# Performance work log

Hardware: AMD Instinct MI355X
Metric: run time of the kernel (lower is better)

## Reference

```python
import jax, jax.numpy as jnp
import numpy as np

NUM_EXPERTS = 8
EMBED_DIM = 1024
BATCH, SEQ = 4, 2048


def setup_inputs() -> dict:
    key = jax.random.key(0)
    k1, k2, k3 = jax.random.split(key, 3)
    E_symb = jax.random.normal(k1, (BATCH, SEQ, EMBED_DIM), dtype=jnp.float32)
    gate_w = jax.random.normal(k2, (EMBED_DIM, NUM_EXPERTS), dtype=jnp.float32) * 0.02
    gate_b = jnp.zeros((NUM_EXPERTS,), dtype=jnp.float32)
    expert_w = jax.random.normal(k3, (NUM_EXPERTS, EMBED_DIM, EMBED_DIM), dtype=jnp.float32) * 0.02
    return {"E_symb": E_symb, "gate_w": gate_w, "gate_b": gate_b,
            "expert_w": expert_w, "k": 2}


def reference(E_symb, gate_w, gate_b, expert_w, k):
    B, S, D = E_symb.shape
    E = expert_w.shape[0]
    x = E_symb.reshape(-1, D)                       # [T, D]
    logits = x @ gate_w + gate_b                    # [T, E]
    probs = jax.nn.softmax(logits.astype(jnp.float32), axis=-1)
    # top-k selection; NOTE: original renormalizes routing_weights but never
    # applies them to expert outputs -> combine is an UNWEIGHTED sum.
    _, sel = jax.lax.top_k(probs, k)                # [T, k]
    mask = jax.nn.one_hot(sel, E, dtype=x.dtype).sum(axis=1)  # [T, E] in {0,1}
    # dense grouped-GEMM then masked combine (replaces per-expert gather/scatter loop)
    y = jnp.einsum('td,edf->tef', x, expert_w)      # [T, E, D]
    out = jnp.einsum('tef,te->tf', y, mask)         # [T, D]
    return out.reshape(B, S, D)
```

## Files before the change

### kernel.cpp

```cpp
#include <hip/hip_runtime.h>
#include <hip/hip_bf16.h>
#include <stdint.h>

#define T_TOK 8192
#define DIM   1024
#define NEXP  8
#define BM    128
#define BN    128
#define BK2   32

typedef __bf16 bf16_t;
typedef bf16_t bf16x8 __attribute__((ext_vector_type(8)));
typedef bf16_t bf16x4 __attribute__((ext_vector_type(4)));
typedef float  f32x4  __attribute__((ext_vector_type(4)));

#define WS_CNT    0
#define CIDX(p)   ((p) << 4)
#define WS_LIST   8192
#define WS_XBF    (4u << 20)
#define WS_W2     (20u << 20)
#define WS_NEED_PSUM ((size_t)76 << 20)

__device__ const int d_PA[28] = {0,0,0,0,0,0,0,1,1,1,1,1,1,2,2,2,2,2,3,3,3,3,4,4,4,5,5,6};
__device__ const int d_PB[28] = {1,2,3,4,5,6,7,2,3,4,5,6,7,3,4,5,6,7,4,5,6,7,5,6,7,6,7,7};

__device__ __forceinline__ void gload16(const void* g, void* l) {
    __builtin_amdgcn_global_load_lds(
        (const __attribute__((address_space(1))) unsigned int*)g,
        (__attribute__((address_space(3))) unsigned int*)l, 16, 0, 0);
}

__device__ __forceinline__ int swz32(int r, int k) {
    return ((r * BK2 + k) * 2) ^ (((r >> 1) & 3) << 4);
}

#define WAITCNT_VM0()   do { asm volatile("s_waitcnt vmcnt(0)" ::: "memory"); \
                             __builtin_amdgcn_sched_barrier(0); } while (0)
#define WAITCNT_VM4()   do { asm volatile("s_waitcnt vmcnt(4)" ::: "memory"); \
                             __builtin_amdgcn_sched_barrier(0); } while (0)
#define WAITCNT_LGKM0() do { asm volatile("s_waitcnt lgkmcnt(0)" ::: "memory"); \
                             __builtin_amdgcn_sched_barrier(0); } while (0)
#define BARRIER()       do { __builtin_amdgcn_s_barrier(); \
                             __builtin_amdgcn_sched_barrier(0); } while (0)

__global__ void zero_cnt(int4* cnt4) {
    cnt4[threadIdx.x] = int4{0, 0, 0, 0};
}

__global__ __launch_bounds__(256) void pre1(const float* __restrict__ x,
                                            const float* __restrict__ gw,
                                            const float* __restrict__ gb,
                                            const float* __restrict__ ew,
                                            bf16_t* __restrict__ xbf,
                                            bf16_t* __restrict__ wt,
                                            int* __restrict__ cnt,
                                            int* __restrict__ list) {
    __shared__ __align__(16) float sh[NEXP * DIM];
    int bx  = blockIdx.x;
    int tid = threadIdx.x;
    if (bx < 1024) {
        float4 gb0 = *(const float4*)gb;
        float4 gb1 = *(const float4*)(gb + 4);
        float gbl[8] = {gb0.x, gb0.y, gb0.z, gb0.w, gb1.x, gb1.y, gb1.z, gb1.w};
        float* gwt = sh;
        const float4* gw4 = (const float4*)gw;
        #pragma unroll
        for (int i = 0; i < 8; i++) {
            int f4 = tid + i * 256;
            float4 v = gw4[f4];
            int d  = f4 >> 1;
            int e0 = (f4 & 1) * 4;
            gwt[(e0 + 0) * DIM + d] = v.x;
            gwt[(e0 + 1) * DIM + d] = v.y;
            gwt[(e0 + 2) * DIM + d] = v.z;
            gwt[(e0 + 3) * DIM + d] = v.w;
        }
        __syncthreads();
        int wid  = tid >> 6;
        int lane = tid & 63;
        const float4* gwt4 = (const float4*)gwt;
        for (int tt = 0; tt < 2; tt++) {
            int t = bx * 8 + wid * 2 + tt;
            const float4* xr4 = (const float4*)(x + (size_t)t * DIM);
            float acc[NEXP] = {};
            #pragma unroll
            for (int j = 0; j < 4; j++) {
                int c4 = j * 64 + lane;
                float4 v = xr4[c4];
                bf16x4 b;
                b[0] = (bf16_t)v.x; b[1] = (bf16_t)v.y;
                b[2] = (bf16_t)v.z; b[3] = (bf16_t)v.w;
                *(bf16x4*)(xbf + (size_t)t * DIM + c4 * 4) = b;
                #pragma unroll
                for (int e = 0; e < NEXP; e++) {
                    float4 g = gwt4[e * 256 + c4];
                    acc[e] += v.x * g.x + v.y * g.y + v.z * g.z + v.w * g.w;
                }
            }
            for (int off = 32; off >= 1; off >>= 1)
                #pragma unroll
                for (int e = 0; e < NEXP; e++)
                    acc[e] += __shfl_xor(acc[e], off, 64);
            if (lane == 0) {
                float logit[NEXP];
                #pragma unroll
                for (int e = 0; e < NEXP; e++) logit[e] = acc[e] + gbl[e];
                int b1 = 0; float best = logit[0];
                for (int e = 1; e < NEXP; e++) if (logit[e] > best) { best = logit[e]; b1 = e; }
                int b2 = -1; float best2 = -3.0e38f;
                for (int e = 0; e < NEXP; e++) {
                    if (e == b1) continue;
                    if (logit[e] > best2) { best2 = logit[e]; b2 = e; }
                }
                int a = min(b1, b2), bb = max(b1, b2);
                int p = a * 8 + bb;
                int pos = atomicAdd(&cnt[CIDX(p)], 1);
                list[p * T_TOK + pos] = t;
            }
        }
    } else {
        int bz  = bx - 1024;
        int g   = bz >> 8;
        int rem = bz & 255;
        int f0  = (rem & 15) * 64;
        int d0  = (rem >> 4) * 64;
        float (*tile)[65] = (float (*)[65])sh;
        const float* s1 = ew + ((size_t)g * DIM + d0) * DIM + f0;
        int fl = (tid & 15) * 4;
        int dl = tid >> 4;
        #pragma unroll
        for (int i = 0; i < 4; i++) {
            int d = dl + i * 16;
            float4 u = *(const float4*)(s1 + (size_t)d * DIM + fl);
            tile[d][fl + 0] = u.x; tile[d][fl + 1] = u.y;
            tile[d][fl + 2] = u.z; tile[d][fl + 3] = u.w;
        }
        __syncthreads();
        bf16_t* dst = wt + ((size_t)g * DIM + f0) * DIM + d0;
        int dl2 = (tid & 7) * 8;
        int fl2 = tid >> 3;
        #pragma unroll
        for (int i = 0; i < 2; i++) {
            int f = fl2 + i * 32;
            bf16x8 o;
            #pragma unroll
            for (int c = 0; c < 8; c++) o[c] = (bf16_t)tile[dl2 + c][f];
            *(bf16x8*)(dst + (size_t)f * DIM + dl2) = o;
        }
    }
}

__global__ __launch_bounds__(256) void pairsum(const bf16_t* __restrict__ wt,
                                               bf16_t* __restrict__ wsum) {
    int bz = blockIdx.x;
    int pk = bz >> 7;
    int cx = bz & 127;
    int tid = threadIdx.x;
    const bf16x8* wa = (const bf16x8*)(wt + (size_t)d_PA[pk] * DIM * DIM);
    const bf16x8* wb = (const bf16x8*)(wt + (size_t)d_PB[pk] * DIM * DIM);
    bf16x8*       wo = (bf16x8*)(wsum + (size_t)pk * DIM * DIM);
    int base = cx * 1024 + tid;
    #pragma unroll
    for (int it = 0; it < 4; it++) {
        int c = base + it * 256;
        bf16x8 u = wa[c], v = wb[c], o;
        #pragma unroll
        for (int i = 0; i < 8; i++) o[i] = (bf16_t)((float)u[i] + (float)v[i]);
        wo[c] = o;
    }
}

template <int PSUM>
__global__ __launch_bounds__(256, 4) void moe_gemm(const bf16_t* __restrict__ xbf,
                                                   const bf16_t* __restrict__ wsrc,
                                                   const int* __restrict__ cnt,
                                                   const int* __restrict__ list,
                                                   float* __restrict__ out) {
    __shared__ __align__(16) bf16_t As[2][BM * BK2];
    __shared__ __align__(16) bf16_t Bs[2][BN * BK2];
    __shared__ int toks[BM];
    __shared__ int s_desc[128];
    __shared__ int s_ntile;
    int tid  = threadIdx.x;
    int lane = tid & 63;
    int wv   = tid >> 6;
    int wm   = wv >> 1, wn = wv & 1;

    if (tid < 64) {
        int c  = cnt[CIDX(tid)];
        int tp = (c + BM - 1) >> 7;
        int pre = 0, tot = 0;
        for (int i = 0; i < 64; i++) {
            int v = __shfl(tp, i, 64);
            if (i < tid) pre += v;
            tot += v;
        }
        for (int j = 0; j < tp; j++)
            s_desc[pre + j] = tid | ((j * BM) << 8);
        if (tid == 0) s_ntile = tot;
    }
    __syncthreads();
    int nwork = s_ntile * (DIM / BN);
    int q = nwork >> 3, r = nwork & 7;
    int xcd  = blockIdx.x & 7;
    int slot = blockIdx.x >> 3;
    int share = q + (xcd < r ? 1 : 0);
    if (slot >= share) return;
    int w = xcd * q + min(xcd, r) + slot;

    int dsc = s_desc[w >> 3];
    int n0  = (w & 7) * BN;
    int p   = dsc & 63;
    int m0  = dsc >> 8;
    int e1  = p >> 3, e2 = p & 7;
    int cp  = cnt[CIDX(p)];
    int valid = min(BM, cp - m0);
    if (tid < BM) toks[tid] = list[p * T_TOK + m0 + min(tid, valid - 1)];
    __syncthreads();

    const bf16_t* asrc[2];
    #pragma unroll
    for (int i = 0; i < 2; i++) {
        int c = i * 256 + tid;
        int rr = c >> 2, js = (c & 3) ^ ((rr >> 1) & 3);
        asrc[i] = xbf + (size_t)toks[rr] * DIM + js * 8;
    }

    f32x4 acc[4][4] = {};
    int lr = lane & 15;
    int lk = (lane >> 4) * 8;

    if (PSUM) {
        const bf16_t* bsrc[2];
        int pk = e1 * 7 - (e1 * (e1 - 1)) / 2 + (e2 - e1 - 1);
        const bf16_t* bb = wsrc + (size_t)pk * DIM * DIM;
        #pragma unroll
        for (int i = 0; i < 2; i++) {
            int c = i * 256 + tid;
            int rr = c >> 2, js = (c & 3) ^ ((rr >> 1) & 3);
            bsrc[i] = bb + (size_t)(n0 + rr) * DIM + js * 8;
        }
        #pragma unroll
        for (int i = 0; i < 2; i++)
            gload16(asrc[i], &As[0][(i * 256 + wv * 64) * 8]);
        #pragma unroll
        for (int i = 0; i < 2; i++)
            gload16(bsrc[i], &Bs[0][(i * 256 + wv * 64) * 8]);

        for (int ks = 0; ks < DIM / BK2; ks++) {
            int cur = ks & 1;
            if (ks < DIM / BK2 - 1) {
                int k1 = (ks + 1) * BK2;
                #pragma unroll
                for (int i = 0; i < 2; i++)
                    gload16(asrc[i] + k1, &As[cur ^ 1][(i * 256 + wv * 64) * 8]);
                #pragma unroll
                for (int i = 0; i < 2; i++)
                    gload16(bsrc[i] + k1, &Bs[cur ^ 1][(i * 256 + wv * 64) * 8]);
                WAITCNT_VM4();
            } else {
                WAITCNT_VM0();
            }
            BARRIER();
            const char* Ab = (const char*)As[cur];
            const char* Bb = (const char*)Bs[cur];
            bf16x8 af[4], bfr[4];
            #pragma unroll
            for (int mf = 0; mf < 4; mf++)
                af[mf] = *(const bf16x8*)(Ab + swz32(wm * 64 + mf * 16 + lr, lk));
            #pragma unroll
            for (int nf = 0; nf < 4; nf++)
                bfr[nf] = *(const bf16x8*)(Bb + swz32(wn * 64 + nf * 16 + lr, lk));
            #pragma unroll
            for (int mf = 0; mf < 4; mf++)
                #pragma unroll
                for (int nf = 0; nf < 4; nf++)
                    acc[mf][nf] = __builtin_amdgcn_mfma_f32_16x16x32_bf16(
                        af[mf], bfr[nf], acc[mf][nf], 0, 0, 0);
            BARRIER();
        }
    } else {
        const bf16_t* wt1 = wsrc + (size_t)e1 * DIM * DIM;
        const bf16_t* wt2 = wsrc + (size_t)e2 * DIM * DIM;
        for (int ks = 0; ks < DIM / BK2; ks++) {
            int k0 = ks * BK2;
            #pragma unroll
            for (int i = 0; i < 2; i++)
                gload16(asrc[i] + k0, &As[0][(i * 256 + wv * 64) * 8]);
            #pragma unroll
            for (int i = 0; i < 2; i++) {
                int c = i * 256 + tid;
                int f = c >> 2, j = c & 3;
                const bf16_t* s1 = wt1 + (size_t)(n0 + f) * DIM + k0 + j * 8;
                const bf16_t* s2 = wt2 + (size_t)(n0 + f) * DIM + k0 + j * 8;
                bf16x8 u = *(const bf16x8*)s1, w2v = *(const bf16x8*)s2, o;
                #pragma unroll
                for (int t = 0; t < 8; t++) o[t] = (bf16_t)((float)u[t] + (float)w2v[t]);
                *(bf16x8*)((char*)Bs[0] + swz32(f, j * 8)) = o;
            }
            WAITCNT_LGKM0();
            WAITCNT_VM0();
            BARRIER();
            const char* Ab = (const char*)As[0];
            const char* Bb = (const char*)Bs[0];
            bf16x8 af[4], bfr[4];
            #pragma unroll
            for (int mf = 0; mf < 4; mf++)
                af[mf] = *(const bf16x8*)(Ab + swz32(wm * 64 + mf * 16 + lr, lk));
            #pragma unroll
            for (int nf = 0; nf < 4; nf++)
                bfr[nf] = *(const bf16x8*)(Bb + swz32(wn * 64 + nf * 16 + lr, lk));
            #pragma unroll
            for (int mf = 0; mf < 4; mf++)
                #pragma unroll
                for (int nf = 0; nf < 4; nf++)
                    acc[mf][nf] = __builtin_amdgcn_mfma_f32_16x16x32_bf16(
                        af[mf], bfr[nf], acc[mf][nf], 0, 0, 0);
            BARRIER();
        }
    }

    #pragma unroll
    for (int mf = 0; mf < 4; mf++) {
        #pragma unroll
        for (int reg = 0; reg < 4; reg++) {
            int rl = wm * 64 + mf * 16 + (lane >> 4) * 4 + reg;
            if (rl < valid) {
                size_t trow = (size_t)toks[rl] * DIM;
                #pragma unroll
                for (int nf = 0; nf < 4; nf++)
                    out[trow + n0 + wn * 64 + nf * 16 + lr] = acc[mf][nf][reg];
            }
        }
    }
}

extern "C" void kernel_launch(void* const* d_in, const int* in_sizes, int n_in,
                              void* d_out, int out_size, void* d_ws, size_t ws_size,
                              hipStream_t stream) {
    const float* x  = (const float*)d_in[0];
    const float* gw = (const float*)d_in[1];
    const float* gb = (const float*)d_in[2];
    const float* ew = (const float*)d_in[3];
    float* out = (float*)d_out;
    char* ws = (char*)d_ws;
    int*    cnt  = (int*)(ws + WS_CNT);
    int*    list = (int*)(ws + WS_LIST);
    bf16_t* xbf  = (bf16_t*)(ws + WS_XBF);
    bf16_t* w2   = (bf16_t*)(ws + WS_W2);
    bool psum = (ws_size >= WS_NEED_PSUM);

    zero_cnt<<<dim3(1), 256, 0, stream>>>((int4*)cnt);
    if (psum) {
        bf16_t* wt_tmp = (bf16_t*)d_out;
        pre1<<<dim3(3072), 256, 0, stream>>>(x, gw, gb, ew, xbf, wt_tmp, cnt, list);
        pairsum<<<dim3(3584), 256, 0, stream>>>(wt_tmp, w2);
        moe_gemm<1><<<dim3(1024), 256, 0, stream>>>(xbf, w2, cnt, list, out);
    } else {
        pre1<<<dim3(3072), 256, 0, stream>>>(x, gw, gb, ew, xbf, w2, cnt, list);
        moe_gemm<0><<<dim3(1024), 256, 0, stream>>>(xbf, w2, cnt, list, out);
    }
}
```

Before: 71.77 us.

## Drop precomputed pair-sum weights; run two MFMA passes per expert in GEMM

Removes the pairsum kernel that built 28 summed expert-weight matrices. The GEMM now streams both experts' weight tiles via async global-to-LDS loads into separate double buffers and issues MFMAs against each. This saves a launch and about 56 MB of pair-sum write traffic, but doubles MFMA work and B-tile loads in the GEMM. It also raises LDS use and lowers the occupancy hint from 4 to 3 blocks.

```diff
diff --git a/kernel.cpp b/kernel.cpp
--- a/kernel.cpp
+++ b/kernel.cpp
@@ -18,11 +18,7 @@
 #define CIDX(p)   ((p) << 4)
 #define WS_LIST   8192
 #define WS_XBF    (4u << 20)
-#define WS_W2     (20u << 20)
-#define WS_NEED_PSUM ((size_t)76 << 20)
-
-__device__ const int d_PA[28] = {0,0,0,0,0,0,0,1,1,1,1,1,1,2,2,2,2,2,3,3,3,3,4,4,4,5,5,6};
-__device__ const int d_PB[28] = {1,2,3,4,5,6,7,2,3,4,5,6,7,3,4,5,6,7,4,5,6,7,5,6,7,6,7,7};
+#define WS_WT     (20u << 20)
 
 __device__ __forceinline__ void gload16(const void* g, void* l) {
     __builtin_amdgcn_global_load_lds(
@@ -36,9 +32,7 @@
 
 #define WAITCNT_VM0()   do { asm volatile("s_waitcnt vmcnt(0)" ::: "memory"); \
                              __builtin_amdgcn_sched_barrier(0); } while (0)
-#define WAITCNT_VM4()   do { asm volatile("s_waitcnt vmcnt(4)" ::: "memory"); \
-                             __builtin_amdgcn_sched_barrier(0); } while (0)
-#define WAITCNT_LGKM0() do { asm volatile("s_waitcnt lgkmcnt(0)" ::: "memory"); \
+#define WAITCNT_VM6()   do { asm volatile("s_waitcnt vmcnt(6)" ::: "memory"); \
                              __builtin_amdgcn_sched_barrier(0); } while (0)
 #define BARRIER()       do { __builtin_amdgcn_s_barrier(); \
                              __builtin_amdgcn_sched_barrier(0); } while (0)
@@ -150,34 +144,14 @@
     }
 }
 
-__global__ __launch_bounds__(256) void pairsum(const bf16_t* __restrict__ wt,
-                                               bf16_t* __restrict__ wsum) {
-    int bz = blockIdx.x;
-    int pk = bz >> 7;
-    int cx = bz & 127;
-    int tid = threadIdx.x;
-    const bf16x8* wa = (const bf16x8*)(wt + (size_t)d_PA[pk] * DIM * DIM);
-    const bf16x8* wb = (const bf16x8*)(wt + (size_t)d_PB[pk] * DIM * DIM);
-    bf16x8*       wo = (bf16x8*)(wsum + (size_t)pk * DIM * DIM);
-    int base = cx * 1024 + tid;
-    #pragma unroll
-    for (int it = 0; it < 4; it++) {
-        int c = base + it * 256;
-        bf16x8 u = wa[c], v = wb[c], o;
-        #pragma unroll
-        for (int i = 0; i < 8; i++) o[i] = (bf16_t)((float)u[i] + (float)v[i]);
-        wo[c] = o;
-    }
-}
-
-template <int PSUM>
-__global__ __launch_bounds__(256, 4) void moe_gemm(const bf16_t* __restrict__ xbf,
-                                                   const bf16_t* __restrict__ wsrc,
-                                                   const int* __restrict__ cnt,
-                                                   const int* __restrict__ list,
-                                                   float* __restrict__ out) {
+__global__ __launch_bounds__(256, 3) void moe_gemm2(const bf16_t* __restrict__ xbf,
+                                                    const bf16_t* __restrict__ wt,
+                                                    const int* __restrict__ cnt,
+                                                    const int* __restrict__ list,
+                                                    float* __restrict__ out) {
     __shared__ __align__(16) bf16_t As[2][BM * BK2];
-    __shared__ __align__(16) bf16_t Bs[2][BN * BK2];
+    __shared__ __align__(16) bf16_t B1[2][BN * BK2];
+    __shared__ __align__(16) bf16_t B2[2][BN * BK2];
     __shared__ int toks[BM];
     __shared__ int s_desc[128];
     __shared__ int s_ntile;
@@ -218,106 +192,71 @@
     if (tid < BM) toks[tid] = list[p * T_TOK + m0 + min(tid, valid - 1)];
     __syncthreads();
 
-    const bf16_t* asrc[2];
+    const bf16_t *asrc[2], *b1src[2], *b2src[2];
+    const bf16_t* w1 = wt + (size_t)e1 * DIM * DIM;
+    const bf16_t* w2 = wt + (size_t)e2 * DIM * DIM;
     #pragma unroll
     for (int i = 0; i < 2; i++) {
         int c = i * 256 + tid;
         int rr = c >> 2, js = (c & 3) ^ ((rr >> 1) & 3);
-        asrc[i] = xbf + (size_t)toks[rr] * DIM + js * 8;
+        asrc[i]  = xbf + (size_t)toks[rr] * DIM + js * 8;
+        b1src[i] = w1 + (size_t)(n0 + rr) * DIM + js * 8;
+        b2src[i] = w2 + (size_t)(n0 + rr) * DIM + js * 8;
     }
 
     f32x4 acc[4][4] = {};
     int lr = lane & 15;
     int lk = (lane >> 4) * 8;
 
-    if (PSUM) {
-        const bf16_t* bsrc[2];
-        int pk = e1 * 7 - (e1 * (e1 - 1)) / 2 + (e2 - e1 - 1);
-        const bf16_t* bb = wsrc + (size_t)pk * DIM * DIM;
-        #pragma unroll
-        for (int i = 0; i < 2; i++) {
-            int c = i * 256 + tid;
-            int rr = c >> 2, js = (c & 3) ^ ((rr >> 1) & 3);
-            bsrc[i] = bb + (size_t)(n0 + rr) * DIM + js * 8;
-        }
-        #pragma unroll
-        for (int i = 0; i < 2; i++)
-            gload16(asrc[i], &As[0][(i * 256 + wv * 64) * 8]);
-        #pragma unroll
-        for (int i = 0; i < 2; i++)
-            gload16(bsrc[i], &Bs[0][(i * 256 + wv * 64) * 8]);
-
-        for (int ks = 0; ks < DIM / BK2; ks++) {
-            int cur = ks & 1;
-            if (ks < DIM / BK2 - 1) {
-                int k1 = (ks + 1) * BK2;
-                #pragma unroll
-                for (int i = 0; i < 2; i++)
-                    gload16(asrc[i] + k1, &As[cur ^ 1][(i * 256 + wv * 64) * 8]);
-                #pragma unroll
-                for (int i = 0; i < 2; i++)
-                    gload16(bsrc[i] + k1, &Bs[cur ^ 1][(i * 256 + wv * 64) * 8]);
-                WAITCNT_VM4();
-            } else {
-                WAITCNT_VM0();
-            }
-            BARRIER();
-            const char* Ab = (const char*)As[cur];
-            const char* Bb = (const char*)Bs[cur];
-            bf16x8 af[4], bfr[4];
-            #pragma unroll
-            for (int mf = 0; mf < 4; mf++)
-                af[mf] = *(const bf16x8*)(Ab + swz32(wm * 64 + mf * 16 + lr, lk));
+    #pragma unroll
+    for (int i = 0; i < 2; i++) {
+        int lds = (i * 256 + wv * 64) * 8;
+        gload16(asrc[i],  &As[0][lds]);
+        gload16(b1src[i], &B1[0][lds]);
+        gload16(b2src[i], &B2[0][lds]);
+    }
+
+    for (int ks = 0; ks < DIM / BK2; ks++) {
+        int cur = ks & 1;
+        if (ks < DIM / BK2 - 1) {
+            int k1 = (ks + 1) * BK2;
+            #pragma unroll
+            for (int i = 0; i < 2; i++) {
+                int lds = (i * 256 + wv * 64) * 8;
+                gload16(asrc[i] + k1,  &As[cur ^ 1][lds]);
+                gload16(b1src[i] + k1, &B1[cur ^ 1][lds]);
+                gload16(b2src[i] + k1, &B2[cur ^ 1][lds]);
+            }
+            WAITCNT_VM6();
+        } else {
+            WAITCNT_VM0();
+        }
+        BARRIER();
+        const char* Ab  = (const char*)As[cur];
+        const char* B1b = (const char*)B1[cur];
+        const char* B2b = (const char*)B2[cur];
+        bf16x8 af[4], b1f[4], b2f[4];
+        #pragma unroll
+        for (int mf = 0; mf < 4; mf++)
+            af[mf] = *(const bf16x8*)(Ab + swz32(wm * 64 + mf * 16 + lr, lk));
+        #pragma unroll
+        for (int nf = 0; nf < 4; nf++) {
+            b1f[nf] = *(const bf16x8*)(B1b + swz32(wn * 64 + nf * 16 + lr, lk));
+            b2f[nf] = *(const bf16x8*)(B2b + swz32(wn * 64 + nf * 16 + lr, lk));
+        }
+        #pragma unroll
+        for (int mf = 0; mf < 4; mf++)
             #pragma unroll
             for (int nf = 0; nf < 4; nf++)
-                bfr[nf] = *(const bf16x8*)(Bb + swz32(wn * 64 + nf * 16 + lr, lk));
-            #pragma unroll
-            for (int mf = 0; mf < 4; mf++)
-                #pragma unroll
-                for (int nf = 0; nf < 4; nf++)
-                    acc[mf][nf] = __builtin_amdgcn_mfma_f32_16x16x32_bf16(
-                        af[mf], bfr[nf], acc[mf][nf], 0, 0, 0);
-            BARRIER();
-        }
-    } else {
-        const bf16_t* wt1 = wsrc + (size_t)e1 * DIM * DIM;
-        const bf16_t* wt2 = wsrc + (size_t)e2 * DIM * DIM;
-        for (int ks = 0; ks < DIM / BK2; ks++) {
-            int k0 = ks * BK2;
-            #pragma unroll
-            for (int i = 0; i < 2; i++)
-                gload16(asrc[i] + k0, &As[0][(i * 256 + wv * 64) * 8]);
-            #pragma unroll
-            for (int i = 0; i < 2; i++) {
-                int c = i * 256 + tid;
-                int f = c >> 2, j = c & 3;
-                const bf16_t* s1 = wt1 + (size_t)(n0 + f) * DIM + k0 + j * 8;
-                const bf16_t* s2 = wt2 + (size_t)(n0 + f) * DIM + k0 + j * 8;
-                bf16x8 u = *(const bf16x8*)s1, w2v = *(const bf16x8*)s2, o;
-                #pragma unroll
-                for (int t = 0; t < 8; t++) o[t] = (bf16_t)((float)u[t] + (float)w2v[t]);
-                *(bf16x8*)((char*)Bs[0] + swz32(f, j * 8)) = o;
-            }
-            WAITCNT_LGKM0();
-            WAITCNT_VM0();
-            BARRIER();
-            const char* Ab = (const char*)As[0];
-            const char* Bb = (const char*)Bs[0];
-            bf16x8 af[4], bfr[4];
-            #pragma unroll
-            for (int mf = 0; mf < 4; mf++)
-                af[mf] = *(const bf16x8*)(Ab + swz32(wm * 64 + mf * 16 + lr, lk));
+                acc[mf][nf] = __builtin_amdgcn_mfma_f32_16x16x32_bf16(
+                    af[mf], b1f[nf], acc[mf][nf], 0, 0, 0);
+        #pragma unroll
+        for (int mf = 0; mf < 4; mf++)
             #pragma unroll
             for (int nf = 0; nf < 4; nf++)
-                bfr[nf] = *(const bf16x8*)(Bb + swz32(wn * 64 + nf * 16 + lr, lk));
-            #pragma unroll
-            for (int mf = 0; mf < 4; mf++)
-                #pragma unroll
-                for (int nf = 0; nf < 4; nf++)
-                    acc[mf][nf] = __builtin_amdgcn_mfma_f32_16x16x32_bf16(
-                        af[mf], bfr[nf], acc[mf][nf], 0, 0, 0);
-            BARRIER();
-        }
+                acc[mf][nf] = __builtin_amdgcn_mfma_f32_16x16x32_bf16(
+                    af[mf], b2f[nf], acc[mf][nf], 0, 0, 0);
+        BARRIER();
     }
 
     #pragma unroll
@@ -347,17 +286,9 @@
     int*    cnt  = (int*)(ws + WS_CNT);
     int*    list = (int*)(ws + WS_LIST);
     bf16_t* xbf  = (bf16_t*)(ws + WS_XBF);
-    bf16_t* w2   = (bf16_t*)(ws + WS_W2);
-    bool psum = (ws_size >= WS_NEED_PSUM);
+    bf16_t* wt   = (bf16_t*)(ws + WS_WT);
 
     zero_cnt<<<dim3(1), 256, 0, stream>>>((int4*)cnt);
-    if (psum) {
-        bf16_t* wt_tmp = (bf16_t*)d_out;
-        pre1<<<dim3(3072), 256, 0, stream>>>(x, gw, gb, ew, xbf, wt_tmp, cnt, list);
-        pairsum<<<dim3(3584), 256, 0, stream>>>(wt_tmp, w2);
-        moe_gemm<1><<<dim3(1024), 256, 0, stream>>>(xbf, w2, cnt, list, out);
-    } else {
-        pre1<<<dim3(3072), 256, 0, stream>>>(x, gw, gb, ew, xbf, w2, cnt, list);
-        moe_gemm<0><<<dim3(1024), 256, 0, stream>>>(xbf, w2, cnt, list, out);
-    }
-}
+    pre1<<<dim3(3072), 256, 0, stream>>>(x, gw, gb, ew, xbf, wt, cnt, list);
+    moe_gemm2<<<dim3(1024), 256, 0, stream>>>(xbf, wt, cnt, list, out);
+}
```

After: 77.71 us. 8.3% more time.
